# Kernel tuning notes

Hardware: AMD Instinct MI355X
Metric: run time of the kernel (lower is better)

The kernel has to match this reference:

```python
import jax, jax.numpy as jnp
import numpy as np

B, M, C = 8, 1024, 768


def setup_inputs() -> dict:
    key = jax.random.key(0)
    ks = jax.random.split(key, 10)
    s = 0.02
    return {
        "layout_x": jax.random.normal(ks[0], (B, M, C), jnp.float32),
        "text_x": jax.random.normal(ks[1], (B, M, C), jnp.float32),
        "mask": jax.random.randint(ks[2], (B, M), 0, 2).astype(jnp.float32),
        "Wqkv": jax.random.normal(ks[3], (C, 3 * C), jnp.float32) * s,
        "bqkv": jnp.zeros((3 * C,), jnp.float32),
        "Wq": jax.random.normal(ks[4], (C, C), jnp.float32) * s,
        "bq": jnp.zeros((C,), jnp.float32),
        "Wkv": jax.random.normal(ks[5], (C, 2 * C), jnp.float32) * s,
        "bkv": jnp.zeros((2 * C,), jnp.float32),
        "Wffn": jax.random.normal(ks[6], (C, C), jnp.float32) * s,
        "bffn": jnp.zeros((C,), jnp.float32),
    }


def _masked_attn(q, k, v, pair_mask, scale):
    # pair_mask: [B,M,M] True where valid (mask_i * mask_j != 0)
    scores = jnp.einsum("bmd,bnd->bmn", q, k) * scale  # [B,M,M]
    scores = jnp.where(pair_mask, scores, jnp.float32(-10000.0))
    attn = jax.nn.softmax(scores, axis=-1)
    return jnp.einsum("bmn,bnd->bmd", attn, v)


def reference(layout_x, text_x, mask, Wqkv, bqkv, Wq, bq, Wkv, bkv, Wffn, bffn):
    dim = layout_x.shape[-1]
    scale = dim ** (-0.5)
    # mask repeated over C then mask@mask.T / C  ==  outer product of 1D masks
    pair = (mask[:, :, None] * mask[:, None, :]) != 0  # [B,M,M] bool, True=keep

    # self-attention on layout_x
    qkv = layout_x @ Wqkv + bqkv  # [B,M,3C]
    q, k, v = jnp.split(qkv, 3, axis=-1)
    layout_o = _masked_attn(q, k, v, pair, scale)

    # cross-attention: q from layout output, k/v from text_x
    cq = layout_o @ Wq + bq
    kv = text_x @ Wkv + bkv  # [B,M,2C]
    ck, cv = jnp.split(kv, 2, axis=-1)
    merge = _masked_attn(cq, ck, cv, pair, scale)

    return merge @ Wffn + bffn
```

## Files before the change

### kernel.cpp

```cpp
#include <hip/hip_runtime.h>
#include <math.h>

#define BDIM 8
#define MDIM 1024
#define CDIM 768
#define ROWS (BDIM * MDIM)

typedef __attribute__((ext_vector_type(8))) short short8;
typedef __attribute__((ext_vector_type(8))) unsigned short ushort8;
typedef __attribute__((ext_vector_type(4))) float f32x4;

#define MFMA16(a, b, c) __builtin_amdgcn_mfma_f32_16x16x32_bf16((a), (b), (c), 0, 0, 0)

#define BAR() __builtin_amdgcn_s_barrier()
#define FENCE() asm volatile("" ::: "memory")
#define SCHED_FENCE() __builtin_amdgcn_sched_barrier(0)
#define WAIT_LGKM0() asm volatile("s_waitcnt lgkmcnt(0)" ::: "memory")
#define WAIT_LGKM4() asm volatile("s_waitcnt lgkmcnt(4)" ::: "memory")
#define WAIT_LGKM8() asm volatile("s_waitcnt lgkmcnt(8)" ::: "memory")
#define WAIT_VM8() asm volatile("s_waitcnt vmcnt(8)" ::: "memory")
#define WAIT_VM6() asm volatile("s_waitcnt vmcnt(6)" ::: "memory")
#define WAIT_VM4() asm volatile("s_waitcnt vmcnt(4)" ::: "memory")
#define WAIT_VM2() asm volatile("s_waitcnt vmcnt(2)" ::: "memory")
#define WAIT_VM0() asm volatile("s_waitcnt vmcnt(0)" ::: "memory")

__device__ __forceinline__ unsigned short f2bf(float f) {
  unsigned u = __float_as_uint(f);
  return (unsigned short)((u + 0x7FFFu + ((u >> 16) & 1u)) >> 16);
}

__device__ __forceinline__ short8 dsr128(unsigned off) {
  short8 r;
  asm volatile("ds_read_b128 %0, %1" : "=v"(r) : "v"(off));
  return r;
}

__global__ __launch_bounds__(256) void prologue(
    const float* __restrict__ xl, const float* __restrict__ xt,
    unsigned short* __restrict__ dxl, unsigned short* __restrict__ dxt,
    const float* __restrict__ W0, const float* __restrict__ W1,
    const float* __restrict__ W2, const float* __restrict__ W3,
    unsigned short* __restrict__ D0, unsigned short* __restrict__ D1,
    unsigned short* __restrict__ D2, unsigned short* __restrict__ D3) {
  const int bx = blockIdx.x;
  const int tid = threadIdx.x;
  if (bx < 6144) {
    const float* src = bx < 3072 ? xl : xt;
    unsigned short* dst = bx < 3072 ? dxl : dxt;
    const int i = ((bx < 3072 ? bx : bx - 3072) * 256 + tid) * 8;
    const float4 a = *(const float4*)(src + i);
    const float4 b = *(const float4*)(src + i + 4);
    ushort8 o;
    o[0] = f2bf(a.x); o[1] = f2bf(a.y); o[2] = f2bf(a.z); o[3] = f2bf(a.w);
    o[4] = f2bf(b.x); o[5] = f2bf(b.y); o[6] = f2bf(b.z); o[7] = f2bf(b.w);
    *(ushort8*)(dst + i) = o;
  } else {
    int x = bx - 6144;
    int bxx = x % 168;
    const int k0 = (x / 168) * 32;
    const float* W; unsigned short* D; int N;
    if (bxx < 72)       { W = W0; D = D0; N = 2304; }
    else if (bxx < 96)  { W = W1; D = D1; N = 768;  bxx -= 72; }
    else if (bxx < 144) { W = W2; D = D2; N = 1536; bxx -= 96; }
    else                { W = W3; D = D3; N = 768;  bxx -= 144; }
    __shared__ unsigned short t[32][33];
    const int tx = tid & 31, ty = tid >> 5;
    const int n0 = bxx * 32;
#pragma unroll
    for (int i = 0; i < 4; ++i)
      t[ty + i * 8][tx] = f2bf(W[(size_t)(k0 + ty + i * 8) * N + n0 + tx]);
    __syncthreads();
#pragma unroll
    for (int i = 0; i < 4; ++i)
      D[(size_t)(n0 + ty + i * 8) * CDIM + k0 + tx] = t[tx][ty + i * 8];
  }
}

template <int J>
__device__ __forceinline__ void stageJ(
    const unsigned short* __restrict__ g, int ld, int k0,
    unsigned short* lds, int wave, int lane) {
  const int gchunk = (lane & 7) ^ (lane >> 3);
#pragma unroll
  for (int j = 0; j < J; ++j) {
    const int grp = wave * J + j;
    const unsigned short* gp =
        g + (size_t)(grp * 8 + (lane >> 3)) * ld + k0 + gchunk * 8;
    __builtin_amdgcn_global_load_lds(
        (const __attribute__((address_space(1))) unsigned int*)gp,
        (__attribute__((address_space(3))) unsigned int*)(lds + grp * 512),
        16, 0, 0);
  }
}

__device__ __forceinline__ void mfma_loop64h(
    const unsigned short* __restrict__ A, int lda,
    const unsigned short* __restrict__ Bt, int ldb, int K,
    unsigned short* As, unsigned short* Bs, f32x4 acc[2][4],
    int wave, int lane) {
  const int wx = wave & 1, wy = wave >> 1;
  const int quad = lane >> 4, l16 = lane & 15;
  for (int k0 = 0; k0 < K; k0 += 64) {
    stageJ<2>(A, lda, k0, As, wave, lane);
    stageJ<4>(Bt, ldb, k0, Bs, wave, lane);
    __syncthreads();
#pragma unroll
    for (int h = 0; h < 2; ++h) {
      const int slot = ((((h << 2) | quad) ^ (l16 & 7))) * 8;
      short8 afr[2], bfr[4];
#pragma unroll
      for (int mt = 0; mt < 2; ++mt)
        afr[mt] = *(const short8*)&As[(wy * 32 + mt * 16 + l16) * 64 + slot];
#pragma unroll
      for (int nt = 0; nt < 4; ++nt)
        bfr[nt] = *(const short8*)&Bs[(wx * 64 + nt * 16 + l16) * 64 + slot];
#pragma unroll
      for (int mt = 0; mt < 2; ++mt)
#pragma unroll
        for (int nt = 0; nt < 4; ++nt)
          acc[mt][nt] = MFMA16(afr[mt], bfr[nt], acc[mt][nt]);
    }
    __syncthreads();
  }
}

#define MFMA_PHASE(GM, GN, AA, BB)                                          \
  do {                                                                      \
    SCHED_FENCE();                                                          \
    __builtin_amdgcn_s_setprio(1);                                          \
    _Pragma("unroll") for (int mf = 0; mf < 4; ++mf)                        \
    _Pragma("unroll") for (int nf = 0; nf < 2; ++nf)                        \
    _Pragma("unroll") for (int kh = 0; kh < 2; ++kh)                        \
        acc[GM][GN][mf][nf] =                                               \
            MFMA16(AA[mf][kh], BB[nf][kh], acc[GM][GN][mf][nf]);            \
    __builtin_amdgcn_s_setprio(0);                                          \
    SCHED_FENCE();                                                          \
  } while (0)

#define RD_A(dst, base)                                                     \
  do {                                                                      \
    _Pragma("unroll") for (int mf = 0; mf < 4; ++mf) {                      \
      dst[mf][0] = dsr128((base) + aRow[mf] + sl0);                         \
      dst[mf][1] = dsr128((base) + aRow[mf] + sl1);                         \
    }                                                                       \
  } while (0)
#define RD_B(dst, base)                                                     \
  do {                                                                      \
    _Pragma("unroll") for (int nf = 0; nf < 2; ++nf) {                      \
      dst[nf][0] = dsr128((base) + bRow[nf] + sl0);                         \
      dst[nf][1] = dsr128((base) + bRow[nf] + sl1);                         \
    }                                                                       \
  } while (0)

__global__ __launch_bounds__(512, 2) void gemm_qkvkv(
    const unsigned short* __restrict__ A0g, const unsigned short* __restrict__ B0g,
    const float* __restrict__ bias0, unsigned short* __restrict__ Y0,
    unsigned short* __restrict__ vT0,
    const unsigned short* __restrict__ A1g, const unsigned short* __restrict__ B1g,
    const float* __restrict__ bias1, unsigned short* __restrict__ Y1,
    unsigned short* __restrict__ vT1) {
  __shared__ __align__(16) unsigned short lds[65536];
  int lin = blockIdx.x;
  const unsigned short *A, *Bt; const float* bias;
  unsigned short *Y, *vTd; int lastSlice, m0, c0;
  if (lin < 288) {
    A = A0g; Bt = B0g; bias = bias0; Y = Y0; vTd = vT0; lastSlice = 2;
    const int xcd = lin & 7, j = lin >> 3;
    m0 = (xcd * 4 + (j & 3)) * 256; c0 = (j >> 2) * 256;
  } else {
    lin -= 288;
    A = A1g; Bt = B1g; bias = bias1; Y = Y1; vTd = vT1; lastSlice = 1;
    const int xcd = lin & 7, j = lin >> 3;
    m0 = (xcd * 4 + (j & 3)) * 256; c0 = (j >> 2) * 256;
  }
  const int tid = threadIdx.x;
  const int wave = tid >> 6, lane = tid & 63;
  const int wy = wave >> 2, wx = wave & 3;
  const int quad = lane >> 4, l16 = lane & 15;

  const unsigned short* Ah[2] = {A + (size_t)m0 * CDIM,
                                 A + (size_t)(m0 + 128) * CDIM};
  const unsigned short* Bh[2] = {Bt + (size_t)c0 * CDIM,
                                 Bt + (size_t)(c0 + 128) * CDIM};

  const unsigned sl0 = (unsigned)((quad ^ (l16 & 7)) * 16);
  const unsigned sl1 = (unsigned)(((4 | quad) ^ (l16 & 7)) * 16);
  unsigned aRow[4], bRow[2];
#pragma unroll
  for (int mf = 0; mf < 4; ++mf)
    aRow[mf] = (unsigned)((wy * 64 + mf * 16 + l16) * 128);
#pragma unroll
  for (int nf = 0; nf < 2; ++nf)
    bRow[nf] = (unsigned)((wx * 32 + nf * 16 + l16) * 128);

  const f32x4 vzero = {0.f, 0.f, 0.f, 0.f};
  f32x4 acc[2][2][4][2];
#pragma unroll
  for (int gm = 0; gm < 2; ++gm)
#pragma unroll
    for (int gn = 0; gn < 2; ++gn)
#pragma unroll
      for (int mf = 0; mf < 4; ++mf)
#pragma unroll
        for (int nf = 0; nf < 2; ++nf) acc[gm][gn][mf][nf] = vzero;
  short8 afrE[4][2], afrO[4][2], b0r[2][2], b1r[2][2];

  stageJ<2>(Ah[0], CDIM, 0, lds + 0, wave, lane);
  stageJ<2>(Bh[0], CDIM, 0, lds + 16384, wave, lane);
  stageJ<2>(Bh[1], CDIM, 0, lds + 24576, wave, lane);
  stageJ<2>(Ah[1], CDIM, 0, lds + 8192, wave, lane);
  stageJ<2>(Ah[0], CDIM, 64, lds + 32768 + 0, wave, lane);
  stageJ<2>(Bh[0], CDIM, 64, lds + 32768 + 16384, wave, lane);
  stageJ<2>(Bh[1], CDIM, 64, lds + 32768 + 24576, wave, lane);
  WAIT_VM8();
  BAR(); FENCE();
  RD_A(afrE, 0u);
  RD_B(b0r, 32768u);

  for (int t = 0; t < 10; ++t) {
    unsigned short* bufcP = lds + (t & 1) * 32768;
    unsigned short* bufnP = lds + ((t + 1) & 1) * 32768;
    const unsigned bc = (unsigned)((t & 1) * 65536);
    const unsigned bn = (unsigned)(((t + 1) & 1) * 65536);
    RD_B(b1r, bc + 49152u);
    stageJ<2>(Ah[1], CDIM, (t + 1) * 64, bufnP + 8192, wave, lane);
    WAIT_VM8(); BAR(); WAIT_LGKM4();
    MFMA_PHASE(0, 0, afrE, b0r);
    RD_A(afrO, bc + 16384u);
    stageJ<2>(Ah[0], CDIM, (t + 2) * 64, bufcP + 0, wave, lane);
    WAIT_VM8(); BAR(); WAIT_LGKM8();
    MFMA_PHASE(0, 1, afrE, b1r);
    RD_A(afrE, bn + 0u);
    stageJ<2>(Bh[0], CDIM, (t + 2) * 64, bufcP + 16384, wave, lane);
    WAIT_VM8(); BAR(); WAIT_LGKM8();
    MFMA_PHASE(1, 0, afrO, b0r);
    RD_B(b0r, bn + 32768u);
    stageJ<2>(Bh[1], CDIM, (t + 2) * 64, bufcP + 24576, wave, lane);
    WAIT_VM8(); BAR();
    MFMA_PHASE(1, 1, afrO, b1r);
  }
  {
    const unsigned bc = 0u, bn = 65536u;
    unsigned short* bufnP = lds + 32768;
    RD_B(b1r, bc + 49152u);
    stageJ<2>(Ah[1], CDIM, 11 * 64, bufnP + 8192, wave, lane);
    WAIT_VM8(); BAR(); WAIT_LGKM4();
    MFMA_PHASE(0, 0, afrE, b0r);

    RD_A(afrO, bc + 16384u);
    WAIT_VM6(); BAR(); WAIT_LGKM8();
    MFMA_PHASE(0, 1, afrE, b1r);

    RD_A(afrE, bn + 0u);
    WAIT_VM4(); BAR(); WAIT_LGKM8();
    MFMA_PHASE(1, 0, afrO, b0r);

    RD_B(b0r, bn + 32768u);
    WAIT_VM2(); BAR();
    MFMA_PHASE(1, 1, afrO, b1r);
  }
  {
    const unsigned bc = 65536u;
    RD_B(b1r, bc + 49152u);
    WAIT_VM0(); BAR(); WAIT_LGKM4();
    MFMA_PHASE(0, 0, afrE, b0r);

    RD_A(afrO, bc + 16384u);
    WAIT_LGKM8();
    MFMA_PHASE(0, 1, afrE, b1r);

    WAIT_LGKM0();
    MFMA_PHASE(1, 0, afrO, b0r);
    MFMA_PHASE(1, 1, afrO, b1r);
  }

#pragma unroll
  for (int gm = 0; gm < 2; ++gm)
#pragma unroll
    for (int gn = 0; gn < 2; ++gn) {
      const int cb2 = c0 + gn * 128 + wx * 32;
      const int slice = cb2 / 768;
      const int rb = m0 + gm * 128 + wy * 64;
      if (slice == lastSlice) {
#pragma unroll
        for (int mf = 0; mf < 4; ++mf) {
          const int row0 = rb + mf * 16 + quad * 4;
          const int b = row0 >> 10, n0 = row0 & 1023;
#pragma unroll
          for (int nf = 0; nf < 2; ++nf) {
            const int gcol = cb2 + nf * 16 + l16;
            const int d = gcol - slice * 768;
            const float bv = bias[gcol];
            uint2 o;
            o.x = (unsigned)f2bf(acc[gm][gn][mf][nf][0] + bv) |
                  ((unsigned)f2bf(acc[gm][gn][mf][nf][1] + bv) << 16);
            o.y = (unsigned)f2bf(acc[gm][gn][mf][nf][2] + bv) |
                  ((unsigned)f2bf(acc[gm][gn][mf][nf][3] + bv) << 16);
            *(uint2*)&vTd[((size_t)b * CDIM + d) * MDIM + n0] = o;
          }
        }
      } else {
        const size_t sbase = (size_t)slice * ROWS * 768;
#pragma unroll
        for (int mf = 0; mf < 4; ++mf)
#pragma unroll
          for (int nf = 0; nf < 2; ++nf) {
            const int gcol = cb2 + nf * 16 + l16;
            const int lcol = gcol - slice * 768;
            const float bv = bias[gcol];
#pragma unroll
            for (int rg = 0; rg < 4; ++rg) {
              const int row = rb + mf * 16 + quad * 4 + rg;
              Y[sbase + (size_t)row * 768 + lcol] =
                  f2bf(acc[gm][gn][mf][nf][rg] + bv);
            }
          }
      }
    }
}

__global__ __launch_bounds__(256, 4) void gemm_proj64(
    const unsigned short* __restrict__ A, const unsigned short* __restrict__ Bt,
    const float* __restrict__ bias, unsigned short* __restrict__ Y) {
  __shared__ __align__(16) unsigned short As[64 * 64];
  __shared__ __align__(16) unsigned short Bs[128 * 64];
  const int lin = blockIdx.x;
  const int xcd = lin & 7, j = lin >> 3;
  const int m0 = (xcd * 16 + (j & 15)) * 64;
  const int c0 = (j >> 4) * 128;
  const int tid = threadIdx.x;
  const int wave = tid >> 6, lane = tid & 63;
  const int wx = wave & 1, wy = wave >> 1;
  const int quad = lane >> 4, l16 = lane & 15;
  const f32x4 vzero = {0.f, 0.f, 0.f, 0.f};
  f32x4 acc[2][4];
#pragma unroll
  for (int mt = 0; mt < 2; ++mt)
#pragma unroll
    for (int nt = 0; nt < 4; ++nt) acc[mt][nt] = vzero;
  mfma_loop64h(A + (size_t)m0 * CDIM, CDIM, Bt + (size_t)c0 * CDIM, CDIM,
               CDIM, As, Bs, acc, wave, lane);
#pragma unroll
  for (int mt = 0; mt < 2; ++mt)
#pragma unroll
    for (int nt = 0; nt < 4; ++nt) {
      const int col = c0 + wx * 64 + nt * 16 + l16;
      const float bv = bias[col];
#pragma unroll
      for (int rg = 0; rg < 4; ++rg) {
        const int row = m0 + wy * 32 + mt * 16 + quad * 4 + rg;
        Y[(size_t)row * 768 + col] = f2bf(acc[mt][nt][rg] + bv);
      }
    }
}

__global__ __launch_bounds__(256, 4) void gemm_ffn64(
    const unsigned short* __restrict__ A, const unsigned short* __restrict__ Bt,
    const float* __restrict__ bias, float* __restrict__ Y) {
  __shared__ __align__(16) unsigned short As[64 * 64];
  __shared__ __align__(16) unsigned short Bs[128 * 64];
  const int lin = blockIdx.x;
  const int xcd = lin & 7, j = lin >> 3;
  const int m0 = (xcd * 16 + (j & 15)) * 64;
  const int c0 = (j >> 4) * 128;
  const int tid = threadIdx.x;
  const int wave = tid >> 6, lane = tid & 63;
  const int wx = wave & 1, wy = wave >> 1;
  const int quad = lane >> 4, l16 = lane & 15;
  const f32x4 vzero = {0.f, 0.f, 0.f, 0.f};
  f32x4 acc[2][4];
#pragma unroll
  for (int mt = 0; mt < 2; ++mt)
#pragma unroll
    for (int nt = 0; nt < 4; ++nt) acc[mt][nt] = vzero;
  mfma_loop64h(A + (size_t)m0 * CDIM, CDIM, Bt + (size_t)c0 * CDIM, CDIM,
               CDIM, As, Bs, acc, wave, lane);
#pragma unroll
  for (int mt = 0; mt < 2; ++mt)
#pragma unroll
    for (int nt = 0; nt < 4; ++nt) {
      const int col = c0 + wx * 64 + nt * 16 + l16;
      const float bv = bias[col];
#pragma unroll
      for (int rg = 0; rg < 4; ++rg) {
        const int row = m0 + wy * 32 + mt * 16 + quad * 4 + rg;
        Y[(size_t)row * 768 + col] = acc[mt][nt][rg] + bv;
      }
    }
}

__global__ __launch_bounds__(256, 4) void gemm_qk64(
    const unsigned short* __restrict__ Qb, const unsigned short* __restrict__ Kb,
    const float* __restrict__ mask, unsigned short* __restrict__ S, float scale,
    float* __restrict__ rsp) {
  __shared__ __align__(16) unsigned short As[64 * 64];
  __shared__ __align__(16) unsigned short Bs[128 * 64];
  const int c0 = blockIdx.x * 128;
  const int m0 = blockIdx.y * 64;
  const int b = blockIdx.z;
  const int tid = threadIdx.x;
  const int wave = tid >> 6, lane = tid & 63;
  const int wx = wave & 1, wy = wave >> 1;
  const int quad = lane >> 4, l16 = lane & 15;

  const f32x4 vzero = {0.f, 0.f, 0.f, 0.f};
  f32x4 acc[2][4];
#pragma unroll
  for (int mt = 0; mt < 2; ++mt)
#pragma unroll
    for (int nt = 0; nt < 4; ++nt) acc[mt][nt] = vzero;

  mfma_loop64h(Qb + ((size_t)b * MDIM + m0) * CDIM, CDIM,
               Kb + ((size_t)b * MDIM + c0) * CDIM, CDIM, CDIM,
               As, Bs, acc, wave, lane);

  const float* maskb = mask + b * MDIM;
  float mrow[2][4], rsum[2][4];
#pragma unroll
  for (int mt = 0; mt < 2; ++mt)
#pragma unroll
    for (int rg = 0; rg < 4; ++rg) {
      mrow[mt][rg] = maskb[m0 + wy * 32 + mt * 16 + quad * 4 + rg];
      rsum[mt][rg] = 0.f;
    }
  unsigned short* Sb = S + (size_t)b * MDIM * MDIM;
#pragma unroll
  for (int nt = 0; nt < 4; ++nt) {
    const int col = c0 + wx * 64 + nt * 16 + l16;
    const float mcol = maskb[col];
#pragma unroll
    for (int mt = 0; mt < 2; ++mt)
#pragma unroll
      for (int rg = 0; rg < 4; ++rg) {
        const int row = m0 + wy * 32 + mt * 16 + quad * 4 + rg;
        const float e = (mrow[mt][rg] * mcol != 0.f)
                            ? __expf(acc[mt][nt][rg] * scale)
                            : 1e-30f;
        Sb[(size_t)row * MDIM + col] = f2bf(e);
        rsum[mt][rg] += e;
      }
  }
  for (int off = 1; off < 16; off <<= 1) {
#pragma unroll
    for (int mt = 0; mt < 2; ++mt)
#pragma unroll
      for (int rg = 0; rg < 4; ++rg)
        rsum[mt][rg] += __shfl_xor(rsum[mt][rg], off, 64);
  }
  if (l16 == 0) {
    float* rs = rsp + ((((size_t)blockIdx.x * 2 + wx) * 8 + b) << 10) +
                m0 + wy * 32;
#pragma unroll
    for (int mt = 0; mt < 2; ++mt)
#pragma unroll
      for (int rg = 0; rg < 4; ++rg)
        rs[mt * 16 + quad * 4 + rg] = rsum[mt][rg];
  }
}

__global__ __launch_bounds__(256, 4) void attn_pv64(
    const unsigned short* __restrict__ P, const unsigned short* __restrict__ vT,
    unsigned short* __restrict__ O, const float* __restrict__ rsp) {
  __shared__ __align__(16) unsigned short As[64 * 64];
  __shared__ __align__(16) unsigned short Bs[128 * 64];
  const int c0 = blockIdx.x * 128;
  const int m0 = blockIdx.y * 64;
  const int b = blockIdx.z;
  const int tid = threadIdx.x;
  const int wave = tid >> 6, lane = tid & 63;
  const int wx = wave & 1, wy = wave >> 1;
  const int quad = lane >> 4, l16 = lane & 15;

  const f32x4 vzero = {0.f, 0.f, 0.f, 0.f};
  f32x4 acc[2][4];
#pragma unroll
  for (int mt = 0; mt < 2; ++mt)
#pragma unroll
    for (int nt = 0; nt < 4; ++nt) acc[mt][nt] = vzero;

  mfma_loop64h(P + ((size_t)b * MDIM + m0) * MDIM, MDIM,
               vT + ((size_t)b * CDIM + c0) * MDIM, MDIM, MDIM,
               As, Bs, acc, wave, lane);

  const float* rsb = rsp + (((size_t)l16 * 8 + b) << 10) + m0 + wy * 32;
  float inv[2][4];
#pragma unroll
  for (int mt = 0; mt < 2; ++mt)
#pragma unroll
    for (int rg = 0; rg < 4; ++rg) {
      float s = rsb[mt * 16 + quad * 4 + rg];
      for (int off = 1; off < 16; off <<= 1) s += __shfl_xor(s, off, 64);
      inv[mt][rg] = 1.f / s;
    }
#pragma unroll
  for (int mt = 0; mt < 2; ++mt)
#pragma unroll
    for (int nt = 0; nt < 4; ++nt)
#pragma unroll
      for (int rg = 0; rg < 4; ++rg) {
        const int row = m0 + wy * 32 + mt * 16 + quad * 4 + rg;
        const int col = c0 + wx * 64 + nt * 16 + l16;
        O[(size_t)(b * MDIM + row) * CDIM + col] =
            f2bf(acc[mt][nt][rg] * inv[mt][rg]);
      }
}

extern "C" void kernel_launch(void* const* d_in, const int* in_sizes, int n_in,
                              void* d_out, int out_size, void* d_ws, size_t ws_size,
                              hipStream_t stream) {
  const float* layout_x = (const float*)d_in[0];
  const float* text_x   = (const float*)d_in[1];
  const float* maskp    = (const float*)d_in[2];
  const float* Wqkv     = (const float*)d_in[3];
  const float* bqkv     = (const float*)d_in[4];
  const float* Wq       = (const float*)d_in[5];
  const float* bq       = (const float*)d_in[6];
  const float* Wkv      = (const float*)d_in[7];
  const float* bkv      = (const float*)d_in[8];
  const float* Wffn     = (const float*)d_in[9];
  const float* bffn     = (const float*)d_in[10];
  float* out = (float*)d_out;
  char* ws = (char*)d_ws;

  const float scale = 1.0f / sqrtf((float)CDIM);

  unsigned short* xlb    = (unsigned short*)(ws);
  unsigned short* xtb    = (unsigned short*)(ws + 12582912);
  unsigned short* Wqkv_t = (unsigned short*)(ws + 25165824);
  unsigned short* Wq_t   = (unsigned short*)(ws + 28704768);
  unsigned short* Wkv_t  = (unsigned short*)(ws + 29884416);
  unsigned short* Wffn_t = (unsigned short*)(ws + 32243712);
  unsigned short* Qb     = (unsigned short*)(ws + 33423360);
  unsigned short* Kb     = (unsigned short*)(ws + 46006272);
  unsigned short* vT     = (unsigned short*)(ws + 58589184);
  unsigned short* S      = (unsigned short*)(ws + 71172096);
  unsigned short* attn1  = xlb;
  unsigned short* cqb    = Qb;
  unsigned short* cK  = (unsigned short*)out;
  unsigned short* cVT = (unsigned short*)out + 6291456;
  float* rsp = (float*)xtb;

  prologue<<<10176, 256, 0, stream>>>(layout_x, text_x, xlb, xtb,
                                      Wqkv, Wq, Wkv, Wffn,
                                      Wqkv_t, Wq_t, Wkv_t, Wffn_t);
  gemm_qkvkv<<<480, 512, 0, stream>>>(xlb, Wqkv_t, bqkv, Qb, vT,
                                      xtb, Wkv_t, bkv, cK, cVT);
  gemm_qk64<<<dim3(8, 16, BDIM), 256, 0, stream>>>(Qb, Kb, maskp, S, scale, rsp);
  attn_pv64<<<dim3(6, 16, BDIM), 256, 0, stream>>>(S, vT, attn1, rsp);
  gemm_proj64<<<768, 256, 0, stream>>>(attn1, Wq_t, bq, cqb);
  gemm_qk64<<<dim3(8, 16, BDIM), 256, 0, stream>>>(cqb, cK, maskp, S, scale, rsp);
  attn_pv64<<<dim3(6, 16, BDIM), 256, 0, stream>>>(S, cVT, attn1, rsp);
  gemm_ffn64<<<768, 256, 0, stream>>>(attn1, Wffn_t, bffn, out);
}
```

Before: 306.1 us.

## Fold output projections into V via precomputed Wv·Wq and Wv·Wffn weights

```diff
diff --git a/kernel.cpp b/kernel.cpp
--- a/kernel.cpp
+++ b/kernel.cpp
@@ -41,7 +41,8 @@
     const float* __restrict__ W0, const float* __restrict__ W1,
     const float* __restrict__ W2, const float* __restrict__ W3,
     unsigned short* __restrict__ D0, unsigned short* __restrict__ D1,
-    unsigned short* __restrict__ D2, unsigned short* __restrict__ D3) {
+    unsigned short* __restrict__ D2, unsigned short* __restrict__ D3,
+    unsigned short* __restrict__ VR0, unsigned short* __restrict__ VR1) {
   const int bx = blockIdx.x;
   const int tid = threadIdx.x;
   if (bx < 6144) {
@@ -54,7 +55,7 @@
     o[0] = f2bf(a.x); o[1] = f2bf(a.y); o[2] = f2bf(a.z); o[3] = f2bf(a.w);
     o[4] = f2bf(b.x); o[5] = f2bf(b.y); o[6] = f2bf(b.z); o[7] = f2bf(b.w);
     *(ushort8*)(dst + i) = o;
-  } else {
+  } else if (bx < 10176) {
     int x = bx - 6144;
     int bxx = x % 168;
     const int k0 = (x / 168) * 32;
@@ -73,6 +74,20 @@
 #pragma unroll
     for (int i = 0; i < 4; ++i)
       D[(size_t)(n0 + ty + i * 8) * CDIM + k0 + tx] = t[tx][ty + i * 8];
+  } else {
+    const int isQ = bx < 10464;
+    const int x = bx - (isQ ? 10176 : 10464);
+    const int i = (x * 256 + tid) * 8;
+    const int row = i / 768, col = i - row * 768;
+    const float* src = isQ ? (W0 + (size_t)row * 2304 + 1536 + col)
+                           : (W2 + (size_t)row * 1536 + 768 + col);
+    unsigned short* dst = (isQ ? VR0 : VR1) + i;
+    const float4 a = *(const float4*)(src);
+    const float4 b = *(const float4*)(src + 4);
+    ushort8 o;
+    o[0] = f2bf(a.x); o[1] = f2bf(a.y); o[2] = f2bf(a.z); o[3] = f2bf(a.w);
+    o[4] = f2bf(b.x); o[5] = f2bf(b.y); o[6] = f2bf(b.z); o[7] = f2bf(b.w);
+    *(ushort8*)(dst) = o;
   }
 }
 
@@ -122,6 +137,60 @@
     }
     __syncthreads();
   }
+}
+
+__global__ __launch_bounds__(256, 4) void wpre(
+    const unsigned short* __restrict__ Wq_t, const unsigned short* __restrict__ VR0,
+    const unsigned short* __restrict__ Wffn_t, const unsigned short* __restrict__ VR1,
+    unsigned short* __restrict__ Wvq_t, unsigned short* __restrict__ Wvf_t,
+    const float* __restrict__ Wq, const float* __restrict__ Wffn,
+    const float* __restrict__ bqkv, const float* __restrict__ bq,
+    const float* __restrict__ bkv, const float* __restrict__ bffn,
+    float* __restrict__ bvq, float* __restrict__ bvf) {
+  const int blk = blockIdx.x;
+  const int tid = threadIdx.x;
+  if (blk >= 144) {
+#pragma unroll
+    for (int rep = 0; rep < 3; ++rep) {
+      const int n = tid + rep * 256;
+      float s1 = bq[n], s2 = bffn[n];
+      for (int c = 0; c < 768; ++c) {
+        s1 += bqkv[1536 + c] * Wq[(size_t)c * 768 + n];
+        s2 += bkv[768 + c] * Wffn[(size_t)c * 768 + n];
+      }
+      bvq[n] = s1; bvf[n] = s2;
+    }
+    return;
+  }
+  __shared__ __align__(16) unsigned short As[64 * 64];
+  __shared__ __align__(16) unsigned short Bs[128 * 64];
+  int g = blk;
+  const unsigned short *A, *Bt; unsigned short* D;
+  if (g < 72) { A = Wq_t; Bt = VR0; D = Wvq_t; }
+  else { g -= 72; A = Wffn_t; Bt = VR1; D = Wvf_t; }
+  const int m0 = (g % 12) * 64, c0 = (g / 12) * 128;
+  const int wave = tid >> 6, lane = tid & 63;
+  const int wx = wave & 1, wy = wave >> 1;
+  const int quad = lane >> 4, l16 = lane & 15;
+  const f32x4 vzero = {0.f, 0.f, 0.f, 0.f};
+  f32x4 acc[2][4];
+#pragma unroll
+  for (int mt = 0; mt < 2; ++mt)
+#pragma unroll
+    for (int nt = 0; nt < 4; ++nt) acc[mt][nt] = vzero;
+  mfma_loop64h(A + (size_t)m0 * CDIM, CDIM, Bt + (size_t)c0 * CDIM, CDIM,
+               CDIM, As, Bs, acc, wave, lane);
+#pragma unroll
+  for (int mt = 0; mt < 2; ++mt)
+#pragma unroll
+    for (int nt = 0; nt < 4; ++nt) {
+      const int col = c0 + wx * 64 + nt * 16 + l16;
+#pragma unroll
+      for (int rg = 0; rg < 4; ++rg) {
+        const int row = m0 + wy * 32 + mt * 16 + quad * 4 + rg;
+        D[(size_t)row * 768 + col] = f2bf(acc[mt][nt][rg]);
+      }
+    }
 }
 
 #define MFMA_PHASE(GM, GN, AA, BB)                                          \
@@ -155,24 +224,31 @@
 __global__ __launch_bounds__(512, 2) void gemm_qkvkv(
     const unsigned short* __restrict__ A0g, const unsigned short* __restrict__ B0g,
     const float* __restrict__ bias0, unsigned short* __restrict__ Y0,
-    unsigned short* __restrict__ vT0,
+    unsigned short* __restrict__ vT0, const unsigned short* __restrict__ Bvw0,
     const unsigned short* __restrict__ A1g, const unsigned short* __restrict__ B1g,
     const float* __restrict__ bias1, unsigned short* __restrict__ Y1,
-    unsigned short* __restrict__ vT1) {
+    unsigned short* __restrict__ vT1, const unsigned short* __restrict__ Bvw1) {
   __shared__ __align__(16) unsigned short lds[65536];
   int lin = blockIdx.x;
-  const unsigned short *A, *Bt; const float* bias;
+  const unsigned short *A, *Bt, *Balt; const float* bias;
   unsigned short *Y, *vTd; int lastSlice, m0, c0;
   if (lin < 288) {
-    A = A0g; Bt = B0g; bias = bias0; Y = Y0; vTd = vT0; lastSlice = 2;
+    A = A0g; Bt = B0g; Balt = Bvw0; bias = bias0; Y = Y0; vTd = vT0;
+    lastSlice = 2;
     const int xcd = lin & 7, j = lin >> 3;
     m0 = (xcd * 4 + (j & 3)) * 256; c0 = (j >> 2) * 256;
   } else {
     lin -= 288;
-    A = A1g; Bt = B1g; bias = bias1; Y = Y1; vTd = vT1; lastSlice = 1;
+    A = A1g; Bt = B1g; Balt = Bvw1; bias = bias1; Y = Y1; vTd = vT1;
+    lastSlice = 1;
     const int xcd = lin & 7, j = lin >> 3;
     m0 = (xcd * 4 + (j & 3)) * 256; c0 = (j >> 2) * 256;
   }
+  const int sw = lastSlice * 768;
+  const unsigned short* Bsel = Bt;
+  int c0b = c0;
+  if (c0 >= sw) { Bsel = Balt; c0b = c0 - sw; }
+
   const int tid = threadIdx.x;
   const int wave = tid >> 6, lane = tid & 63;
   const int wy = wave >> 2, wx = wave & 3;
@@ -180,8 +256,8 @@
 
   const unsigned short* Ah[2] = {A + (size_t)m0 * CDIM,
                                  A + (size_t)(m0 + 128) * CDIM};
-  const unsigned short* Bh[2] = {Bt + (size_t)c0 * CDIM,
-                                 Bt + (size_t)(c0 + 128) * CDIM};
+  const unsigned short* Bh[2] = {Bsel + (size_t)c0b * CDIM,
+                                 Bsel + (size_t)(c0b + 128) * CDIM};
 
   const unsigned sl0 = (unsigned)((quad ^ (l16 & 7)) * 16);
   const unsigned sl1 = (unsigned)(((4 | quad) ^ (l16 & 7)) * 16);
@@ -290,12 +366,11 @@
           for (int nf = 0; nf < 2; ++nf) {
             const int gcol = cb2 + nf * 16 + l16;
             const int d = gcol - slice * 768;
-            const float bv = bias[gcol];
             uint2 o;
-            o.x = (unsigned)f2bf(acc[gm][gn][mf][nf][0] + bv) |
-                  ((unsigned)f2bf(acc[gm][gn][mf][nf][1] + bv) << 16);
-            o.y = (unsigned)f2bf(acc[gm][gn][mf][nf][2] + bv) |
-                  ((unsigned)f2bf(acc[gm][gn][mf][nf][3] + bv) << 16);
+            o.x = (unsigned)f2bf(acc[gm][gn][mf][nf][0]) |
+                  ((unsigned)f2bf(acc[gm][gn][mf][nf][1]) << 16);
+            o.y = (unsigned)f2bf(acc[gm][gn][mf][nf][2]) |
+                  ((unsigned)f2bf(acc[gm][gn][mf][nf][3]) << 16);
             *(uint2*)&vTd[((size_t)b * CDIM + d) * MDIM + n0] = o;
           }
         }
@@ -315,76 +390,6 @@
                   f2bf(acc[gm][gn][mf][nf][rg] + bv);
             }
           }
-      }
-    }
-}
-
-__global__ __launch_bounds__(256, 4) void gemm_proj64(
-    const unsigned short* __restrict__ A, const unsigned short* __restrict__ Bt,
-    const float* __restrict__ bias, unsigned short* __restrict__ Y) {
-  __shared__ __align__(16) unsigned short As[64 * 64];
-  __shared__ __align__(16) unsigned short Bs[128 * 64];
-  const int lin = blockIdx.x;
-  const int xcd = lin & 7, j = lin >> 3;
-  const int m0 = (xcd * 16 + (j & 15)) * 64;
-  const int c0 = (j >> 4) * 128;
-  const int tid = threadIdx.x;
-  const int wave = tid >> 6, lane = tid & 63;
-  const int wx = wave & 1, wy = wave >> 1;
-  const int quad = lane >> 4, l16 = lane & 15;
-  const f32x4 vzero = {0.f, 0.f, 0.f, 0.f};
-  f32x4 acc[2][4];
-#pragma unroll
-  for (int mt = 0; mt < 2; ++mt)
-#pragma unroll
-    for (int nt = 0; nt < 4; ++nt) acc[mt][nt] = vzero;
-  mfma_loop64h(A + (size_t)m0 * CDIM, CDIM, Bt + (size_t)c0 * CDIM, CDIM,
-               CDIM, As, Bs, acc, wave, lane);
-#pragma unroll
-  for (int mt = 0; mt < 2; ++mt)
-#pragma unroll
-    for (int nt = 0; nt < 4; ++nt) {
-      const int col = c0 + wx * 64 + nt * 16 + l16;
-      const float bv = bias[col];
-#pragma unroll
-      for (int rg = 0; rg < 4; ++rg) {
-        const int row = m0 + wy * 32 + mt * 16 + quad * 4 + rg;
-        Y[(size_t)row * 768 + col] = f2bf(acc[mt][nt][rg] + bv);
-      }
-    }
-}
-
-__global__ __launch_bounds__(256, 4) void gemm_ffn64(
-    const unsigned short* __restrict__ A, const unsigned short* __restrict__ Bt,
-    const float* __restrict__ bias, float* __restrict__ Y) {
-  __shared__ __align__(16) unsigned short As[64 * 64];
-  __shared__ __align__(16) unsigned short Bs[128 * 64];
-  const int lin = blockIdx.x;
-  const int xcd = lin & 7, j = lin >> 3;
-  const int m0 = (xcd * 16 + (j & 15)) * 64;
-  const int c0 = (j >> 4) * 128;
-  const int tid = threadIdx.x;
-  const int wave = tid >> 6, lane = tid & 63;
-  const int wx = wave & 1, wy = wave >> 1;
-  const int quad = lane >> 4, l16 = lane & 15;
-  const f32x4 vzero = {0.f, 0.f, 0.f, 0.f};
-  f32x4 acc[2][4];
-#pragma unroll
-  for (int mt = 0; mt < 2; ++mt)
-#pragma unroll
-    for (int nt = 0; nt < 4; ++nt) acc[mt][nt] = vzero;
-  mfma_loop64h(A + (size_t)m0 * CDIM, CDIM, Bt + (size_t)c0 * CDIM, CDIM,
-               CDIM, As, Bs, acc, wave, lane);
-#pragma unroll
-  for (int mt = 0; mt < 2; ++mt)
-#pragma unroll
-    for (int nt = 0; nt < 4; ++nt) {
-      const int col = c0 + wx * 64 + nt * 16 + l16;
-      const float bv = bias[col];
-#pragma unroll
-      for (int rg = 0; rg < 4; ++rg) {
-        const int row = m0 + wy * 32 + mt * 16 + quad * 4 + rg;
-        Y[(size_t)row * 768 + col] = acc[mt][nt][rg] + bv;
       }
     }
 }
@@ -460,7 +465,8 @@
 
 __global__ __launch_bounds__(256, 4) void attn_pv64(
     const unsigned short* __restrict__ P, const unsigned short* __restrict__ vT,
-    unsigned short* __restrict__ O, const float* __restrict__ rsp) {
+    unsigned short* __restrict__ Ob, float* __restrict__ Of,
+    const float* __restrict__ rsp, const float* __restrict__ bias) {
   __shared__ __align__(16) unsigned short As[64 * 64];
   __shared__ __align__(16) unsigned short Bs[128 * 64];
   const int c0 = blockIdx.x * 128;
@@ -495,14 +501,17 @@
 #pragma unroll
   for (int mt = 0; mt < 2; ++mt)
 #pragma unroll
-    for (int nt = 0; nt < 4; ++nt)
+    for (int nt = 0; nt < 4; ++nt) {
+      const int col = c0 + wx * 64 + nt * 16 + l16;
+      const float bv = bias[col];
 #pragma unroll
       for (int rg = 0; rg < 4; ++rg) {
         const int row = m0 + wy * 32 + mt * 16 + quad * 4 + rg;
-        const int col = c0 + wx * 64 + nt * 16 + l16;
-        O[(size_t)(b * MDIM + row) * CDIM + col] =
-            f2bf(acc[mt][nt][rg] * inv[mt][rg]);
+        const float v = acc[mt][nt][rg] * inv[mt][rg] + bv;
+        if (Of) Of[(size_t)(b * MDIM + row) * CDIM + col] = v;
+        else Ob[(size_t)(b * MDIM + row) * CDIM + col] = f2bf(v);
       }
+    }
 }
 
 extern "C" void kernel_launch(void* const* d_in, const int* in_sizes, int n_in,
@@ -524,31 +533,37 @@
 
   const float scale = 1.0f / sqrtf((float)CDIM);
 
-  unsigned short* xlb    = (unsigned short*)(ws);
-  unsigned short* xtb    = (unsigned short*)(ws + 12582912);
-  unsigned short* Wqkv_t = (unsigned short*)(ws + 25165824);
-  unsigned short* Wq_t   = (unsigned short*)(ws + 28704768);
-  unsigned short* Wkv_t  = (unsigned short*)(ws + 29884416);
-  unsigned short* Wffn_t = (unsigned short*)(ws + 32243712);
-  unsigned short* Qb     = (unsigned short*)(ws + 33423360);
-  unsigned short* Kb     = (unsigned short*)(ws + 46006272);
-  unsigned short* vT     = (unsigned short*)(ws + 58589184);
-  unsigned short* S      = (unsigned short*)(ws + 71172096);
-  unsigned short* attn1  = xlb;
-  unsigned short* cqb    = Qb;
-  unsigned short* cK  = (unsigned short*)out;
-  unsigned short* cVT = (unsigned short*)out + 6291456;
+  unsigned short* xlb     = (unsigned short*)(ws);
+  unsigned short* xtb     = (unsigned short*)(ws + 12582912);
+  unsigned short* Wqkv_t  = (unsigned short*)(ws + 25165824);
+  unsigned short* Wq_t    = (unsigned short*)(ws + 28704768);
+  unsigned short* Wkv_t   = (unsigned short*)(ws + 29884416);
+  unsigned short* Wffn_t  = (unsigned short*)(ws + 32243712);
+  unsigned short* Wvq_t   = (unsigned short*)(ws + 33423360);
+  unsigned short* Wvf_t   = (unsigned short*)(ws + 34603008);
+  unsigned short* Qb      = (unsigned short*)(ws + 35782656);
+  unsigned short* Kb      = (unsigned short*)(ws + 48365568);
+  unsigned short* VWT     = (unsigned short*)(ws + 60948480);
+  unsigned short* cK      = (unsigned short*)(ws + 73531392);
+  unsigned short* cVFT    = (unsigned short*)(ws + 86114304);
+  unsigned short* S       = (unsigned short*)(ws + 98697216);
+  float*          bvq     = (float*)(ws + 115474432);
+  float*          bvf     = (float*)(ws + 115477504);
+  unsigned short* Wqkv_vr = (unsigned short*)(ws + 115480576);
+  unsigned short* Wkv_vr  = (unsigned short*)(ws + 116660224);
+  unsigned short* cqb     = Qb;
   float* rsp = (float*)xtb;
 
-  prologue<<<10176, 256, 0, stream>>>(layout_x, text_x, xlb, xtb,
+  prologue<<<10752, 256, 0, stream>>>(layout_x, text_x, xlb, xtb,
                                       Wqkv, Wq, Wkv, Wffn,
-                                      Wqkv_t, Wq_t, Wkv_t, Wffn_t);
-  gemm_qkvkv<<<480, 512, 0, stream>>>(xlb, Wqkv_t, bqkv, Qb, vT,
-                                      xtb, Wkv_t, bkv, cK, cVT);
+                                      Wqkv_t, Wq_t, Wkv_t, Wffn_t,
+                                      Wqkv_vr, Wkv_vr);
+  wpre<<<145, 256, 0, stream>>>(Wq_t, Wqkv_vr, Wffn_t, Wkv_vr, Wvq_t, Wvf_t,
+                                Wq, Wffn, bqkv, bq, bkv, bffn, bvq, bvf);
+  gemm_qkvkv<<<480, 512, 0, stream>>>(xlb, Wqkv_t, bqkv, Qb, VWT, Wvq_t,
+                                      xtb, Wkv_t, bkv, cK, cVFT, Wvf_t);
   gemm_qk64<<<dim3(8, 16, BDIM), 256, 0, stream>>>(Qb, Kb, maskp, S, scale, rsp);
-  attn_pv64<<<dim3(6, 16, BDIM), 256, 0, stream>>>(S, vT, attn1, rsp);
-  gemm_proj64<<<768, 256, 0, stream>>>(attn1, Wq_t, bq, cqb);
+  attn_pv64<<<dim3(6, 16, BDIM), 256, 0, stream>>>(S, VWT, cqb, nullptr, rsp, bvq);
   gemm_qk64<<<dim3(8, 16, BDIM), 256, 0, stream>>>(cqb, cK, maskp, S, scale, rsp);
-  attn_pv64<<<dim3(6, 16, BDIM), 256, 0, stream>>>(S, cVT, attn1, rsp);
-  gemm_ffn64<<<768, 256, 0, stream>>>(attn1, Wffn_t, bffn, out);
-}
+  attn_pv64<<<dim3(6, 16, BDIM), 256, 0, stream>>>(S, cVFT, nullptr, out, rsp, bvf);
+}
```

Result: slower. 416.6 us (+36.1%).
